# Performance work log

Measured on AMD Instinct MI355X. Metric: run time of the kernel, lower is better.

The kernel has to match this reference:

```python
import jax, jax.numpy as jnp
import numpy as np

B, N, C = 32, 577, 768
H = 12
D = C // H
HID = 4 * C
EPS = 1e-5


def setup_inputs() -> dict:
    key = jax.random.key(0)
    ks = jax.random.split(key, 12)
    s = 0.02
    return {
        "x": jax.random.normal(ks[0], (B, N, C), dtype=jnp.float32),
        "ln1_g": jnp.ones((C,), jnp.float32),
        "ln1_b": jnp.zeros((C,), jnp.float32),
        "qkv_w": jax.random.normal(ks[1], (C, 3 * C), jnp.float32) * s,
        "qkv_b": jnp.zeros((3 * C,), jnp.float32),
        "proj_w": jax.random.normal(ks[2], (C, C), jnp.float32) * s,
        "proj_b": jnp.zeros((C,), jnp.float32),
        "ln2_g": jnp.ones((C,), jnp.float32),
        "ln2_b": jnp.zeros((C,), jnp.float32),
        "fc1_w": jax.random.normal(ks[3], (C, HID), jnp.float32) * s,
        "fc1_b": jnp.zeros((HID,), jnp.float32),
        "fc2_w": jax.random.normal(ks[4], (HID, C), jnp.float32) * s,
        "fc2_b": jnp.zeros((C,), jnp.float32),
    }


def _layernorm(x, g, b):
    mu = jnp.mean(x, axis=-1, keepdims=True)
    var = jnp.mean(jnp.square(x - mu), axis=-1, keepdims=True)
    return (x - mu) * jax.lax.rsqrt(var + EPS) * g + b


def reference(x, ln1_g, ln1_b, qkv_w, qkv_b, proj_w, proj_b,
              ln2_g, ln2_b, fc1_w, fc1_b, fc2_w, fc2_b):
    b, n, c = x.shape
    # --- MSA branch ---
    h = _layernorm(x, ln1_g, ln1_b)
    qkv = h @ qkv_w + qkv_b                      # [b, n, 3c]
    qkv = qkv.reshape(b, n, 3, H, D).transpose(2, 0, 3, 1, 4)  # [3, b, h, n, d]
    q, k, v = qkv[0], qkv[1], qkv[2]
    scale = D ** -0.5
    attn = jnp.einsum('bhqd,bhkd->bhqk', q, k) * scale
    attn = jax.nn.softmax(attn, axis=-1)
    o = jnp.einsum('bhqk,bhkd->bhqd', attn, v)   # [b, h, n, d]
    o = o.transpose(0, 2, 1, 3).reshape(b, n, c)
    o = o @ proj_w + proj_b
    x = x + o
    # --- MLP branch ---
    h = _layernorm(x, ln2_g, ln2_b)
    h = jax.nn.gelu(h @ fc1_w + fc1_b, approximate=False)  # torch nn.GELU = exact erf
    h = h @ fc2_w + fc2_b
    return x + h
```

## Files before the change

### kernel.cpp

```cpp
#include <hip/hip_runtime.h>

typedef unsigned short u16;
typedef short short8 __attribute__((ext_vector_type(8)));
typedef float f32x4 __attribute__((ext_vector_type(4)));

#define MM 18464
#define NTOK 577

__device__ __forceinline__ u16 f2bf(float f) {
    unsigned u = __builtin_bit_cast(unsigned, f);
    u += 0x7fffu + ((u >> 16) & 1u);
    return (u16)(u >> 16);
}

__device__ __forceinline__ void gload16(const void* g, void* lds) {
    __builtin_amdgcn_global_load_lds(
        (const __attribute__((address_space(1))) unsigned*)g,
        (__attribute__((address_space(3))) unsigned*)lds,
        16, 0, 0);
}

__device__ __forceinline__ int xcd_map(int flat, int nwg) {
    const int q = nwg >> 3, r = nwg & 7;
    const int xcd = flat & 7, lid = flat >> 3;
    return (xcd < r ? xcd * (q + 1) : r * (q + 1) + (xcd - r) * q) + lid;
}

__device__ __forceinline__ int2 xcd_swz2(int gx, int gy) {
    const int w = xcd_map(blockIdx.x + blockIdx.y * gx, gx * gy);
    int2 o; o.x = w % gx; o.y = w / gx; return o;
}

__global__ __launch_bounds__(256) void convT(const float* __restrict__ src,
                                             u16* __restrict__ dst, int K, int N) {
    __shared__ float tile[32][33];
    const int k0 = blockIdx.x * 32, n0 = blockIdx.y * 32;
    const int tx = threadIdx.x & 31, ty = threadIdx.x >> 5;
#pragma unroll
    for (int i = 0; i < 32; i += 8)
        tile[ty + i][tx] = src[(size_t)(k0 + ty + i) * N + n0 + tx];
    __syncthreads();
#pragma unroll
    for (int i = 0; i < 32; i += 8)
        dst[(size_t)(n0 + ty + i) * K + k0 + tx] = f2bf(tile[tx][ty + i]);
}

__global__ __launch_bounds__(192) void ln_k(const float* __restrict__ x,
                                            const float* __restrict__ g,
                                            const float* __restrict__ bt,
                                            u16* __restrict__ out) {
    const int row = blockIdx.x, t = threadIdx.x;
    const float4 v = reinterpret_cast<const float4*>(x + (size_t)row * 768)[t];
    float s = v.x + v.y + v.z + v.w;
    float s2 = v.x * v.x + v.y * v.y + v.z * v.z + v.w * v.w;
#pragma unroll
    for (int off = 32; off > 0; off >>= 1) {
        s += __shfl_down(s, off);
        s2 += __shfl_down(s2, off);
    }
    __shared__ float red[6];
    if ((t & 63) == 0) { red[t >> 6] = s; red[3 + (t >> 6)] = s2; }
    __syncthreads();
    const float S = red[0] + red[1] + red[2];
    const float S2 = red[3] + red[4] + red[5];
    const float mu = S * (1.f / 768.f);
    const float var = S2 * (1.f / 768.f) - mu * mu;
    const float rs = rsqrtf(var + 1e-5f);
    const float4 gg = reinterpret_cast<const float4*>(g)[t];
    const float4 bb = reinterpret_cast<const float4*>(bt)[t];
    ushort4 r;
    r.x = f2bf((v.x - mu) * rs * gg.x + bb.x);
    r.y = f2bf((v.y - mu) * rs * gg.y + bb.y);
    r.z = f2bf((v.z - mu) * rs * gg.z + bb.z);
    r.w = f2bf((v.w - mu) * rs * gg.w + bb.w);
    reinterpret_cast<ushort4*>(out + (size_t)row * 768)[t] = r;
}

template <int MODE>
__global__ __launch_bounds__(512, 2) void gemm_k(const u16* __restrict__ A,
                                                 const u16* __restrict__ BT,
                                                 const float* __restrict__ bias,
                                                 const float* __restrict__ resid,
                                                 void* __restrict__ outp,
                                                 int M, int N, int K, int mt) {
    __shared__ u16 smem[4][256 * 64];
    const int t = threadIdx.x;
    const int wid = t >> 6, lane = t & 63;
    const int l15 = lane & 15, lg = lane >> 4;
    const int wr = wid >> 2, wc = wid & 3;

    const int w = xcd_map(blockIdx.x, gridDim.x);
    const int m0 = (w % mt) * 256, n0 = (w / mt) * 256;

    f32x4 acc[8][4] = {};
    const int NT = K >> 6;

    auto stage = [&](int buf, int k0) {
        u16* Ad = smem[buf * 2];
        u16* Bd = smem[buf * 2 + 1];
#pragma unroll
        for (int i = 0; i < 4; ++i) {
            const int slot = i * 512 + t;
            const int r = slot >> 3, sl = slot & 7;
            const int cs = (sl ^ (r & 7)) << 3;
            const size_t dofs = (size_t)(i * 512 + (t & ~63)) * 8;
            gload16(A + (size_t)min(m0 + r, M - 1) * K + k0 + cs, Ad + dofs);
            gload16(BT + (size_t)(n0 + r) * K + k0 + cs, Bd + dofs);
        }
    };

    auto compute = [&](int buf) {
        const u16* Ab = smem[buf * 2];
        const u16* Bb = smem[buf * 2 + 1];
#pragma unroll
        for (int half = 0; half < 2; ++half) {
            short8 af[8], bf4[4];
#pragma unroll
            for (int mf = 0; mf < 8; ++mf) {
                const int r = wr * 128 + mf * 16 + l15;
                af[mf] = *(const short8*)&Ab[r * 64 + (((half * 4 + lg) ^ (l15 & 7)) << 3)];
            }
#pragma unroll
            for (int nf = 0; nf < 4; ++nf) {
                const int r = wc * 64 + nf * 16 + l15;
                bf4[nf] = *(const short8*)&Bb[r * 64 + (((half * 4 + lg) ^ (l15 & 7)) << 3)];
            }
            __builtin_amdgcn_s_setprio(1);
#pragma unroll
            for (int mf = 0; mf < 8; ++mf)
#pragma unroll
                for (int nf = 0; nf < 4; ++nf)
                    acc[mf][nf] = __builtin_amdgcn_mfma_f32_16x16x32_bf16(
                        af[mf], bf4[nf], acc[mf][nf], 0, 0, 0);
            __builtin_amdgcn_s_setprio(0);
        }
    };

    stage(0, 0);
    stage(1, 64);
    for (int tt = 0; tt < NT; ++tt) {
        if (tt < NT - 1) asm volatile("s_waitcnt vmcnt(8)" ::: "memory");
        else             asm volatile("s_waitcnt vmcnt(0)" ::: "memory");
        __builtin_amdgcn_s_barrier();
        __builtin_amdgcn_sched_barrier(0);
        compute(tt & 1);
        __builtin_amdgcn_sched_barrier(0);
        asm volatile("s_waitcnt lgkmcnt(0)" ::: "memory");
        __builtin_amdgcn_s_barrier();
        __builtin_amdgcn_sched_barrier(0);
        if (tt + 2 < NT) stage(tt & 1, (tt + 2) << 6);
    }

    float bcol[4];
#pragma unroll
    for (int nf = 0; nf < 4; ++nf) bcol[nf] = bias[n0 + wc * 64 + nf * 16 + l15];
#pragma unroll
    for (int mf = 0; mf < 8; ++mf) {
#pragma unroll
        for (int reg = 0; reg < 4; ++reg) {
            const int row = m0 + wr * 128 + mf * 16 + lg * 4 + reg;
            if (row < M) {
#pragma unroll
                for (int nf = 0; nf < 4; ++nf) {
                    const int col = n0 + wc * 64 + nf * 16 + l15;
                    float v = acc[mf][nf][reg] + bcol[nf];
                    if (MODE == 2) v = 0.5f * v * (1.0f + erff(v * 0.70710678118f));
                    if (MODE == 1 || MODE == 3) v += resid[(size_t)row * N + col];
                    if (MODE == 0 || MODE == 2)
                        ((u16*)outp)[(size_t)row * N + col] = f2bf(v);
                    else
                        ((float*)outp)[(size_t)row * N + col] = v;
                }
            }
        }
    }
}

__global__ __launch_bounds__(256) void attn_k(const u16* __restrict__ qkv,
                                              u16* __restrict__ o) {
    const int2 sw = xcd_swz2(10, 384);
    const int qt = sw.x;
    const int bh = sw.y;
    const int b = bh / 12, h = bh % 12;
    const int t = threadIdx.x, wid = t >> 6, lane = t & 63;
    const int l15 = lane & 15, lg = lane >> 4;
    const size_t base = ((size_t)b * NTOK) * 2304 + (size_t)h * 64;

    __shared__ u16 Ks[64 * 64], VT[64 * 64], Ps[64 * 64];

    int qrow = qt * 64 + wid * 16 + l15;
    qrow = min(qrow, NTOK - 1);
    const u16* Qp = qkv + base + (size_t)qrow * 2304 + lg * 8;
    const short8 qf0 = *(const short8*)(Qp);
    const short8 qf1 = *(const short8*)(Qp + 32);

    f32x4 oacc[4] = {};
    float m_run[4], l_run[4];
#pragma unroll
    for (int j = 0; j < 4; ++j) { m_run[j] = -1e30f; l_run[j] = 0.f; }

    const int srow = t >> 3;
    const int cchunk = t & 7;
    const int ksd = (cchunk ^ (srow & 7)) * 8;
    u16* ldsK = Ks + wid * 512;
    const int vs0 = ((srow >> 3) ^ cchunk) * 8 + (srow & 7);
    const int vs1 = (((srow >> 3) + 4) ^ cchunk) * 8 + (srow & 7);

    for (int kt = 0; kt < 10; ++kt) {
        const int n0t = kt * 64;
        const int r0 = min(n0t + srow, NTOK - 1);
        const int r1 = min(n0t + srow + 32, NTOK - 1);
        gload16(qkv + base + 768 + (size_t)r0 * 2304 + ksd, ldsK);
        gload16(qkv + base + 768 + (size_t)r1 * 2304 + ksd, ldsK + 2048);
        const short8 v0 = *(const short8*)(qkv + base + 1536 + (size_t)r0 * 2304 + cchunk * 8);
        const short8 v1 = *(const short8*)(qkv + base + 1536 + (size_t)r1 * 2304 + cchunk * 8);
#pragma unroll
        for (int j = 0; j < 8; ++j) {
            VT[(cchunk * 8 + j) * 64 + vs0] = (u16)v0[j];
            VT[(cchunk * 8 + j) * 64 + vs1] = (u16)v1[j];
        }
        __syncthreads();

        f32x4 s[4];
#pragma unroll
        for (int fc = 0; fc < 4; ++fc) {
            const int krow = fc * 16 + l15;
            const short8 kf0 = *(const short8*)&Ks[krow * 64 + ((lg ^ (krow & 7)) * 8)];
            const short8 kf1 = *(const short8*)&Ks[krow * 64 + (((lg + 4) ^ (krow & 7)) * 8)];
            f32x4 a_ = {};
            a_ = __builtin_amdgcn_mfma_f32_16x16x32_bf16(qf0, kf0, a_, 0, 0, 0);
            a_ = __builtin_amdgcn_mfma_f32_16x16x32_bf16(qf1, kf1, a_, 0, 0, 0);
            s[fc] = a_;
        }
#pragma unroll
        for (int fc = 0; fc < 4; ++fc) {
            const bool valid = (n0t + fc * 16 + l15) < NTOK;
#pragma unroll
            for (int j = 0; j < 4; ++j)
                s[fc][j] = valid ? s[fc][j] * 0.125f : -1e30f;
        }
        float mt_[4];
#pragma unroll
        for (int j = 0; j < 4; ++j)
            mt_[j] = fmaxf(fmaxf(s[0][j], s[1][j]), fmaxf(s[2][j], s[3][j]));
#pragma unroll
        for (int off = 1; off < 16; off <<= 1)
#pragma unroll
            for (int j = 0; j < 4; ++j) mt_[j] = fmaxf(mt_[j], __shfl_xor(mt_[j], off));
        float mn[4], alpha[4];
#pragma unroll
        for (int j = 0; j < 4; ++j) {
            mn[j] = fmaxf(m_run[j], mt_[j]);
            alpha[j] = __expf(m_run[j] - mn[j]);
            m_run[j] = mn[j];
        }
        float lsum[4] = {0.f, 0.f, 0.f, 0.f};
#pragma unroll
        for (int fc = 0; fc < 4; ++fc)
#pragma unroll
            for (int j = 0; j < 4; ++j) {
                const float p = __expf(s[fc][j] - mn[j]);
                s[fc][j] = p;
                lsum[j] += p;
            }
#pragma unroll
        for (int off = 1; off < 16; off <<= 1)
#pragma unroll
            for (int j = 0; j < 4; ++j) lsum[j] += __shfl_xor(lsum[j], off);
#pragma unroll
        for (int j = 0; j < 4; ++j) l_run[j] = l_run[j] * alpha[j] + lsum[j];
#pragma unroll
        for (int fc = 0; fc < 4; ++fc)
#pragma unroll
            for (int j = 0; j < 4; ++j) oacc[fc][j] *= alpha[j];

#pragma unroll
        for (int fc = 0; fc < 4; ++fc)
#pragma unroll
            for (int j = 0; j < 4; ++j) {
                const int q = wid * 16 + lg * 4 + j;
                Ps[q * 64 + (((fc * 2 + (l15 >> 3)) ^ (q & 7)) * 8) + (l15 & 7)] =
                    f2bf(s[fc][j]);
            }
        asm volatile("s_waitcnt lgkmcnt(0)" ::: "memory");

#pragma unroll
        for (int c = 0; c < 2; ++c) {
            const short8 pf = *(const short8*)
                &Ps[(wid * 16 + l15) * 64 + (((c * 4 + lg) ^ (l15 & 7)) * 8)];
#pragma unroll
            for (int fc = 0; fc < 4; ++fc) {
                const short8 vf = *(const short8*)
                    &VT[(fc * 16 + l15) * 64 +
                        (((c * 4 + lg) ^ (fc * 2 + (l15 >> 3))) * 8)];
                oacc[fc] = __builtin_amdgcn_mfma_f32_16x16x32_bf16(pf, vf, oacc[fc], 0, 0, 0);
            }
        }
        __syncthreads();
    }

#pragma unroll
    for (int j = 0; j < 4; ++j) {
        const int row = qt * 64 + wid * 16 + lg * 4 + j;
        if (row < NTOK) {
            const float inv = 1.0f / l_run[j];
#pragma unroll
            for (int fc = 0; fc < 4; ++fc)
                o[((size_t)(b * NTOK + row)) * 768 + h * 64 + fc * 16 + l15] =
                    f2bf(oacc[fc][j] * inv);
        }
    }
}

extern "C" void kernel_launch(void* const* d_in, const int* in_sizes, int n_in,
                              void* d_out, int out_size, void* d_ws, size_t ws_size,
                              hipStream_t stream) {
    const float* x      = (const float*)d_in[0];
    const float* ln1_g  = (const float*)d_in[1];
    const float* ln1_b  = (const float*)d_in[2];
    const float* qkv_w  = (const float*)d_in[3];
    const float* qkv_b  = (const float*)d_in[4];
    const float* proj_w = (const float*)d_in[5];
    const float* proj_b = (const float*)d_in[6];
    const float* ln2_g  = (const float*)d_in[7];
    const float* ln2_b  = (const float*)d_in[8];
    const float* fc1_w  = (const float*)d_in[9];
    const float* fc1_b  = (const float*)d_in[10];
    const float* fc2_w  = (const float*)d_in[11];
    const float* fc2_b  = (const float*)d_in[12];
    float* out = (float*)d_out;

    char* ws = (char*)d_ws;
    size_t off = 0;
    u16* WQ  = (u16*)(ws + off); off += (size_t)2304 * 768 * 2;
    u16* WP  = (u16*)(ws + off); off += (size_t)768 * 768 * 2;
    u16* W1  = (u16*)(ws + off); off += (size_t)3072 * 768 * 2;
    u16* W2  = (u16*)(ws + off); off += (size_t)768 * 3072 * 2;
    u16* LN1 = (u16*)(ws + off); off += (size_t)MM * 768 * 2;
    u16* QKV = (u16*)(ws + off); off += (size_t)MM * 2304 * 2;
    u16* OB  = (u16*)(ws + off); off += (size_t)MM * 768 * 2;
    float* X1 = (float*)(ws + off); off += (size_t)MM * 768 * 4;
    u16* LN2 = (u16*)(ws + off); off += (size_t)MM * 768 * 2;
    u16* HID = LN1;

    convT<<<dim3(24, 72), 256, 0, stream>>>(qkv_w, WQ, 768, 2304);
    convT<<<dim3(24, 24), 256, 0, stream>>>(proj_w, WP, 768, 768);
    convT<<<dim3(24, 96), 256, 0, stream>>>(fc1_w, W1, 768, 3072);
    convT<<<dim3(96, 24), 256, 0, stream>>>(fc2_w, W2, 3072, 768);

    const int mt = (MM + 255) / 256;
    ln_k<<<MM, 192, 0, stream>>>(x, ln1_g, ln1_b, LN1);
    gemm_k<0><<<mt * 9, 512, 0, stream>>>(LN1, WQ, qkv_b, nullptr, QKV,
                                          MM, 2304, 768, mt);
    attn_k<<<dim3(10, 384), 256, 0, stream>>>(QKV, OB);
    gemm_k<1><<<mt * 3, 512, 0, stream>>>(OB, WP, proj_b, x, X1,
                                          MM, 768, 768, mt);
    ln_k<<<MM, 192, 0, stream>>>(X1, ln2_g, ln2_b, LN2);
    gemm_k<2><<<mt * 12, 512, 0, stream>>>(LN2, W1, fc1_b, nullptr, HID,
                                           MM, 3072, 768, mt);
    gemm_k<3><<<mt * 3, 512, 0, stream>>>(HID, W2, fc2_b, X1, out,
                                          MM, 768, 3072, mt);
}
```

Baseline: 749.6 us.

## Split GEMM k-tiles into half-planes with 4-phase interleaved load/compute pipeline

Restructures the bf16 GEMM main loop so each 64-wide k-tile is held as two 32-wide half planes per matrix. Each tile is processed in four phases, and every phase issues the global-to-LDS prefetch for the next tile while running MFMAs on the current one. The LDS swizzle is changed, and the MFMA operand order is swapped so each lane holds four consecutive output columns. That lets the epilogue use vectorized float4 bias and residual loads and ushort4/float4 stores. The cost is more barriers per tile and more complex wait-count bookkeeping.

Result: no change. 741.6 us (-1.1%).

```diff
diff --git a/kernel.cpp b/kernel.cpp
--- a/kernel.cpp
+++ b/kernel.cpp
@@ -83,93 +83,119 @@
                                                  const float* __restrict__ resid,
                                                  void* __restrict__ outp,
                                                  int M, int N, int K, int mt) {
-    __shared__ u16 smem[4][256 * 64];
+    __shared__ u16 smem[65536];
     const int t = threadIdx.x;
     const int wid = t >> 6, lane = t & 63;
     const int l15 = lane & 15, lg = lane >> 4;
     const int wr = wid >> 2, wc = wid & 3;
-
     const int w = xcd_map(blockIdx.x, gridDim.x);
     const int m0 = (w % mt) * 256, n0 = (w / mt) * 256;
+    const int swz = (l15 >> 1) & 3;
 
     f32x4 acc[8][4] = {};
     const int NT = K >> 6;
 
-    auto stage = [&](int buf, int k0) {
-        u16* Ad = smem[buf * 2];
-        u16* Bd = smem[buf * 2 + 1];
-#pragma unroll
-        for (int i = 0; i < 4; ++i) {
-            const int slot = i * 512 + t;
-            const int r = slot >> 3, sl = slot & 7;
-            const int cs = (sl ^ (r & 7)) << 3;
-            const size_t dofs = (size_t)(i * 512 + (t & ~63)) * 8;
-            gload16(A + (size_t)min(m0 + r, M - 1) * K + k0 + cs, Ad + dofs);
-            gload16(BT + (size_t)(n0 + r) * K + k0 + cs, Bd + dofs);
+    auto stage = [&](int buf, int kt, int mat, int kh) {
+        u16* plane = smem + (size_t)(((buf << 1) | mat) * 2 + kh) * 8192;
+        const u16* src = mat ? BT : A;
+        const int rbase = mat ? n0 : m0;
+        const int kk = kt * 64 + kh * 32;
+#pragma unroll
+        for (int i = 0; i < 2; ++i) {
+            const int flat = i * 512 + t;
+            const int r = flat >> 2, c = flat & 3;
+            const int scol = (c ^ ((r >> 1) & 3)) << 3;
+            int grow = rbase + r;
+            if (mat == 0) grow = min(grow, M - 1);
+            gload16(src + (size_t)grow * K + kk + scol,
+                    plane + (size_t)(i * 512 + (t & ~63)) * 8);
         }
     };
 
-    auto compute = [&](int buf) {
-        const u16* Ab = smem[buf * 2];
-        const u16* Bb = smem[buf * 2 + 1];
-#pragma unroll
-        for (int half = 0; half < 2; ++half) {
-            short8 af[8], bf4[4];
-#pragma unroll
-            for (int mf = 0; mf < 8; ++mf) {
-                const int r = wr * 128 + mf * 16 + l15;
-                af[mf] = *(const short8*)&Ab[r * 64 + (((half * 4 + lg) ^ (l15 & 7)) << 3)];
-            }
-#pragma unroll
-            for (int nf = 0; nf < 4; ++nf) {
-                const int r = wc * 64 + nf * 16 + l15;
-                bf4[nf] = *(const short8*)&Bb[r * 64 + (((half * 4 + lg) ^ (l15 & 7)) << 3)];
-            }
-            __builtin_amdgcn_s_setprio(1);
-#pragma unroll
-            for (int mf = 0; mf < 8; ++mf)
-#pragma unroll
-                for (int nf = 0; nf < 4; ++nf)
-                    acc[mf][nf] = __builtin_amdgcn_mfma_f32_16x16x32_bf16(
-                        af[mf], bf4[nf], acc[mf][nf], 0, 0, 0);
-            __builtin_amdgcn_s_setprio(0);
-        }
+    short8 bfv[4];
+    auto read_bf = [&](int buf, int kh) {
+        const u16* plane = smem + (size_t)((buf << 1 | 1) * 2 + kh) * 8192;
+        const int rb = wc * 64 + l15;
+#pragma unroll
+        for (int nf = 0; nf < 4; ++nf)
+            bfv[nf] = *(const short8*)&plane[(rb + nf * 16) * 32 + ((lg ^ swz) << 3)];
     };
-
-    stage(0, 0);
-    stage(1, 64);
-    for (int tt = 0; tt < NT; ++tt) {
-        if (tt < NT - 1) asm volatile("s_waitcnt vmcnt(8)" ::: "memory");
-        else             asm volatile("s_waitcnt vmcnt(0)" ::: "memory");
+    auto phase = [&](int buf, int mh, int kh, bool loadB,
+                     int stMat, int stKh, int kt1, bool doStage, int vm) {
+        if (loadB) read_bf(buf, kh);
+        short8 afv[4];
+        {
+            const u16* plane = smem + (size_t)((buf << 1) * 2 + kh) * 8192;
+            const int rb = wr * 128 + mh * 64 + l15;
+#pragma unroll
+            for (int mf = 0; mf < 4; ++mf)
+                afv[mf] = *(const short8*)&plane[(rb + mf * 16) * 32 + ((lg ^ swz) << 3)];
+        }
+        if (doStage) stage(buf ^ 1, kt1, stMat, stKh);
+        __builtin_amdgcn_s_barrier();
+        asm volatile("s_waitcnt lgkmcnt(0)" ::: "memory");
+        __builtin_amdgcn_sched_barrier(0);
+        __builtin_amdgcn_s_setprio(1);
+#pragma unroll
+        for (int mf = 0; mf < 4; ++mf)
+#pragma unroll
+            for (int nf = 0; nf < 4; ++nf)
+                acc[mh * 4 + mf][nf] = __builtin_amdgcn_mfma_f32_16x16x32_bf16(
+                    bfv[nf], afv[mf], acc[mh * 4 + mf][nf], 0, 0, 0);
+        __builtin_amdgcn_s_setprio(0);
+        if (vm == 4)      asm volatile("s_waitcnt vmcnt(4)" ::: "memory");
+        else if (vm == 0) asm volatile("s_waitcnt vmcnt(0)" ::: "memory");
         __builtin_amdgcn_s_barrier();
         __builtin_amdgcn_sched_barrier(0);
-        compute(tt & 1);
-        __builtin_amdgcn_sched_barrier(0);
-        asm volatile("s_waitcnt lgkmcnt(0)" ::: "memory");
-        __builtin_amdgcn_s_barrier();
-        __builtin_amdgcn_sched_barrier(0);
-        if (tt + 2 < NT) stage(tt & 1, (tt + 2) << 6);
-    }
-
-    float bcol[4];
-#pragma unroll
-    for (int nf = 0; nf < 4; ++nf) bcol[nf] = bias[n0 + wc * 64 + nf * 16 + l15];
+    };
+
+    stage(0, 0, 0, 0); stage(0, 0, 1, 0); stage(0, 0, 0, 1); stage(0, 0, 1, 1);
+    asm volatile("s_waitcnt vmcnt(4)" ::: "memory");
+    __builtin_amdgcn_s_barrier();
+    __builtin_amdgcn_sched_barrier(0);
+
+    int buf = 0;
+    for (int tt = 0; tt < NT; ++tt) {
+        const bool pre = (tt + 1 < NT);
+        phase(buf, 0, 0, true,  0, 0, tt + 1, pre, -1);
+        phase(buf, 1, 0, false, 1, 0, tt + 1, pre, pre ? 4 : 0);
+        phase(buf, 0, 1, true,  0, 1, tt + 1, pre, -1);
+        phase(buf, 1, 1, false, 1, 1, tt + 1, pre, pre ? 4 : -1);
+        buf ^= 1;
+    }
+
+    float4 bb4[4];
+#pragma unroll
+    for (int nf = 0; nf < 4; ++nf)
+        bb4[nf] = *(const float4*)&bias[n0 + wc * 64 + nf * 16 + lg * 4];
 #pragma unroll
     for (int mf = 0; mf < 8; ++mf) {
-#pragma unroll
-        for (int reg = 0; reg < 4; ++reg) {
-            const int row = m0 + wr * 128 + mf * 16 + lg * 4 + reg;
-            if (row < M) {
-#pragma unroll
-                for (int nf = 0; nf < 4; ++nf) {
-                    const int col = n0 + wc * 64 + nf * 16 + l15;
-                    float v = acc[mf][nf][reg] + bcol[nf];
-                    if (MODE == 2) v = 0.5f * v * (1.0f + erff(v * 0.70710678118f));
-                    if (MODE == 1 || MODE == 3) v += resid[(size_t)row * N + col];
-                    if (MODE == 0 || MODE == 2)
-                        ((u16*)outp)[(size_t)row * N + col] = f2bf(v);
-                    else
-                        ((float*)outp)[(size_t)row * N + col] = v;
+        const int row = m0 + wr * 128 + mf * 16 + l15;
+        if (row < M) {
+#pragma unroll
+            for (int nf = 0; nf < 4; ++nf) {
+                const int col = n0 + wc * 64 + nf * 16 + lg * 4;
+                float v0 = acc[mf][nf][0] + bb4[nf].x;
+                float v1 = acc[mf][nf][1] + bb4[nf].y;
+                float v2 = acc[mf][nf][2] + bb4[nf].z;
+                float v3 = acc[mf][nf][3] + bb4[nf].w;
+                if (MODE == 2) {
+                    v0 = 0.5f * v0 * (1.0f + erff(v0 * 0.70710678118f));
+                    v1 = 0.5f * v1 * (1.0f + erff(v1 * 0.70710678118f));
+                    v2 = 0.5f * v2 * (1.0f + erff(v2 * 0.70710678118f));
+                    v3 = 0.5f * v3 * (1.0f + erff(v3 * 0.70710678118f));
+                }
+                if (MODE == 1 || MODE == 3) {
+                    const float4 rr = *(const float4*)&resid[(size_t)row * N + col];
+                    v0 += rr.x; v1 += rr.y; v2 += rr.z; v3 += rr.w;
+                }
+                if (MODE == 0 || MODE == 2) {
+                    ushort4 r4;
+                    r4.x = f2bf(v0); r4.y = f2bf(v1); r4.z = f2bf(v2); r4.w = f2bf(v3);
+                    *(ushort4*)&((u16*)outp)[(size_t)row * N + col] = r4;
+                } else {
+                    float4 f4; f4.x = v0; f4.y = v1; f4.z = v2; f4.w = v3;
+                    *(float4*)&((float*)outp)[(size_t)row * N + col] = f4;
                 }
             }
         }
```

## Restructure GEMM main loop into half-K stages with interleaved prefetch and LDS epilogue

Applied to the files above, without the earlier changes.

Rewrites the GEMM mainloop so each 64-wide K tile is split into two 32-wide sub-tiles, with global-to-LDS prefetch of the next tile issued between MFMA groups instead of after a full barrier. Precomputed load pointers and a new swizzle cut address arithmetic, and the A/B operand order in the MFMA is swapped. The epilogue now transposes accumulators through padded LDS, so bias, GELU, residual and stores use float4/ushort4 vector accesses instead of scalar ones. The goal is better overlap of memory and matrix work and coalesced stores, at the cost of more complex synchronization and a risk of LDS hazards.

After: 817.7 us. 9.1% more time.

```diff
diff --git a/kernel.cpp b/kernel.cpp
--- a/kernel.cpp
+++ b/kernel.cpp
@@ -83,93 +83,156 @@
                                                  const float* __restrict__ resid,
                                                  void* __restrict__ outp,
                                                  int M, int N, int K, int mt) {
-    __shared__ u16 smem[4][256 * 64];
+    __shared__ u16 smem[65536];
     const int t = threadIdx.x;
     const int wid = t >> 6, lane = t & 63;
     const int l15 = lane & 15, lg = lane >> 4;
     const int wr = wid >> 2, wc = wid & 3;
-
     const int w = xcd_map(blockIdx.x, gridDim.x);
     const int m0 = (w % mt) * 256, n0 = (w / mt) * 256;
+    const int swz = (l15 >> 1) & 3;
+
+    const int rs = t >> 2;
+    const int scol = ((t & 3) ^ ((rs >> 1) & 3)) << 3;
+    const u16* aP0 = A + (size_t)min(m0 + rs, M - 1) * K + scol;
+    const u16* aP1 = A + (size_t)min(m0 + rs + 128, M - 1) * K + scol;
+    const u16* bP0 = BT + (size_t)(n0 + rs) * K + scol;
+    const u16* bP1 = BT + (size_t)(n0 + rs + 128) * K + scol;
+    const int d0 = (t & ~63) * 8, d1 = 4096 + (t & ~63) * 8;
+
+    const int aRd = (wr * 128 + l15) * 32 + ((lg ^ swz) << 3);
+    const int bRd = (wc * 64 + l15) * 32 + ((lg ^ swz) << 3);
 
     f32x4 acc[8][4] = {};
     const int NT = K >> 6;
 
-    auto stage = [&](int buf, int k0) {
-        u16* Ad = smem[buf * 2];
-        u16* Bd = smem[buf * 2 + 1];
-#pragma unroll
-        for (int i = 0; i < 4; ++i) {
-            const int slot = i * 512 + t;
-            const int r = slot >> 3, sl = slot & 7;
-            const int cs = (sl ^ (r & 7)) << 3;
-            const size_t dofs = (size_t)(i * 512 + (t & ~63)) * 8;
-            gload16(A + (size_t)min(m0 + r, M - 1) * K + k0 + cs, Ad + dofs);
-            gload16(BT + (size_t)(n0 + r) * K + k0 + cs, Bd + dofs);
-        }
+    auto stA = [&](int pb, int kk) {
+        gload16(aP0 + kk, smem + pb + d0);
+        gload16(aP1 + kk, smem + pb + d1);
     };
-
-    auto compute = [&](int buf) {
-        const u16* Ab = smem[buf * 2];
-        const u16* Bb = smem[buf * 2 + 1];
-#pragma unroll
-        for (int half = 0; half < 2; ++half) {
-            short8 af[8], bf4[4];
-#pragma unroll
-            for (int mf = 0; mf < 8; ++mf) {
-                const int r = wr * 128 + mf * 16 + l15;
-                af[mf] = *(const short8*)&Ab[r * 64 + (((half * 4 + lg) ^ (l15 & 7)) << 3)];
-            }
-#pragma unroll
-            for (int nf = 0; nf < 4; ++nf) {
-                const int r = wc * 64 + nf * 16 + l15;
-                bf4[nf] = *(const short8*)&Bb[r * 64 + (((half * 4 + lg) ^ (l15 & 7)) << 3)];
-            }
-            __builtin_amdgcn_s_setprio(1);
-#pragma unroll
-            for (int mf = 0; mf < 8; ++mf)
-#pragma unroll
-                for (int nf = 0; nf < 4; ++nf)
-                    acc[mf][nf] = __builtin_amdgcn_mfma_f32_16x16x32_bf16(
-                        af[mf], bf4[nf], acc[mf][nf], 0, 0, 0);
-            __builtin_amdgcn_s_setprio(0);
-        }
+    auto stB = [&](int pb, int kk) {
+        gload16(bP0 + kk, smem + pb + d0);
+        gload16(bP1 + kk, smem + pb + d1);
     };
 
-    stage(0, 0);
-    stage(1, 64);
-    for (int tt = 0; tt < NT; ++tt) {
-        if (tt < NT - 1) asm volatile("s_waitcnt vmcnt(8)" ::: "memory");
-        else             asm volatile("s_waitcnt vmcnt(0)" ::: "memory");
+    auto tile = [&](int pb, int kkn, bool pre, bool last) {
+        short8 bfv[4], afv[4];
+#pragma unroll
+        for (int nf = 0; nf < 4; ++nf)
+            bfv[nf] = *(const short8*)&smem[pb + 16384 + bRd + nf * 512];
+#pragma unroll
+        for (int mf = 0; mf < 4; ++mf)
+            afv[mf] = *(const short8*)&smem[pb + aRd + mf * 512];
+        if (pre) stA(pb ^ 32768, kkn);
+        __builtin_amdgcn_s_setprio(1);
+#pragma unroll
+        for (int mf = 0; mf < 4; ++mf)
+#pragma unroll
+            for (int nf = 0; nf < 4; ++nf)
+                acc[mf][nf] = __builtin_amdgcn_mfma_f32_16x16x32_bf16(
+                    bfv[nf], afv[mf], acc[mf][nf], 0, 0, 0);
+        __builtin_amdgcn_s_setprio(0);
+#pragma unroll
+        for (int mf = 0; mf < 4; ++mf)
+            afv[mf] = *(const short8*)&smem[pb + aRd + 2048 + mf * 512];
+        if (pre) stB((pb ^ 32768) + 16384, kkn);
+        __builtin_amdgcn_s_setprio(1);
+#pragma unroll
+        for (int mf = 0; mf < 4; ++mf)
+#pragma unroll
+            for (int nf = 0; nf < 4; ++nf)
+                acc[4 + mf][nf] = __builtin_amdgcn_mfma_f32_16x16x32_bf16(
+                    bfv[nf], afv[mf], acc[4 + mf][nf], 0, 0, 0);
+        __builtin_amdgcn_s_setprio(0);
+        if (last) asm volatile("s_waitcnt vmcnt(0)" ::: "memory");
+        else      asm volatile("s_waitcnt vmcnt(4)" ::: "memory");
         __builtin_amdgcn_s_barrier();
         __builtin_amdgcn_sched_barrier(0);
-        compute(tt & 1);
-        __builtin_amdgcn_sched_barrier(0);
+#pragma unroll
+        for (int nf = 0; nf < 4; ++nf)
+            bfv[nf] = *(const short8*)&smem[pb + 16384 + 8192 + bRd + nf * 512];
+#pragma unroll
+        for (int mf = 0; mf < 4; ++mf)
+            afv[mf] = *(const short8*)&smem[pb + 8192 + aRd + mf * 512];
+        if (pre) stA((pb ^ 32768) + 8192, kkn + 32);
+        __builtin_amdgcn_s_setprio(1);
+#pragma unroll
+        for (int mf = 0; mf < 4; ++mf)
+#pragma unroll
+            for (int nf = 0; nf < 4; ++nf)
+                acc[mf][nf] = __builtin_amdgcn_mfma_f32_16x16x32_bf16(
+                    bfv[nf], afv[mf], acc[mf][nf], 0, 0, 0);
+        __builtin_amdgcn_s_setprio(0);
+#pragma unroll
+        for (int mf = 0; mf < 4; ++mf)
+            afv[mf] = *(const short8*)&smem[pb + 8192 + aRd + 2048 + mf * 512];
+        if (pre) stB((pb ^ 32768) + 16384 + 8192, kkn + 32);
+        __builtin_amdgcn_s_setprio(1);
+#pragma unroll
+        for (int mf = 0; mf < 4; ++mf)
+#pragma unroll
+            for (int nf = 0; nf < 4; ++nf)
+                acc[4 + mf][nf] = __builtin_amdgcn_mfma_f32_16x16x32_bf16(
+                    bfv[nf], afv[mf], acc[4 + mf][nf], 0, 0, 0);
+        __builtin_amdgcn_s_setprio(0);
+        if (pre) {
+            asm volatile("s_waitcnt vmcnt(4)" ::: "memory");
+            __builtin_amdgcn_s_barrier();
+            __builtin_amdgcn_sched_barrier(0);
+        }
+    };
+
+    stA(0, 0); stB(16384, 0);
+    __builtin_amdgcn_sched_barrier(0);
+    stA(8192, 32); stB(16384 + 8192, 32);
+    asm volatile("s_waitcnt vmcnt(4)" ::: "memory");
+    __builtin_amdgcn_s_barrier();
+    __builtin_amdgcn_sched_barrier(0);
+
+    int kkn = 64;
+    const int half = NT >> 1;
+    for (int it = 0; it < half; ++it) {
+        tile(0, kkn, true, false);
+        kkn += 64;
+        const bool pre = (it + 1 < half);
+        tile(32768, kkn, pre, !pre);
+        kkn += 64;
+    }
+
+    __syncthreads();
+    const int col = n0 + wc * 64 + l15 * 4;
+    const float4 bias4 = *(const float4*)&bias[col];
+#pragma unroll
+    for (int mf = 0; mf < 8; ++mf) {
+        float* ws_ = (float*)smem + wid * 2144 + (mf & 1) * 1072;
         asm volatile("s_waitcnt lgkmcnt(0)" ::: "memory");
-        __builtin_amdgcn_s_barrier();
-        __builtin_amdgcn_sched_barrier(0);
-        if (tt + 2 < NT) stage(tt & 1, (tt + 2) << 6);
-    }
-
-    float bcol[4];
-#pragma unroll
-    for (int nf = 0; nf < 4; ++nf) bcol[nf] = bias[n0 + wc * 64 + nf * 16 + l15];
-#pragma unroll
-    for (int mf = 0; mf < 8; ++mf) {
-#pragma unroll
-        for (int reg = 0; reg < 4; ++reg) {
-            const int row = m0 + wr * 128 + mf * 16 + lg * 4 + reg;
-            if (row < M) {
-#pragma unroll
-                for (int nf = 0; nf < 4; ++nf) {
-                    const int col = n0 + wc * 64 + nf * 16 + l15;
-                    float v = acc[mf][nf][reg] + bcol[nf];
-                    if (MODE == 2) v = 0.5f * v * (1.0f + erff(v * 0.70710678118f));
-                    if (MODE == 1 || MODE == 3) v += resid[(size_t)row * N + col];
-                    if (MODE == 0 || MODE == 2)
-                        ((u16*)outp)[(size_t)row * N + col] = f2bf(v);
-                    else
-                        ((float*)outp)[(size_t)row * N + col] = v;
+#pragma unroll
+        for (int nf = 0; nf < 4; ++nf)
+            *(f32x4*)&ws_[l15 * 67 + nf * 16 + lg * 4] = acc[mf][nf];
+#pragma unroll
+        for (int ps = 0; ps < 4; ++ps) {
+            const int rl = ps * 4 + lg;
+            float4 v = *(const float4*)&ws_[rl * 67 + l15 * 4];
+            v.x += bias4.x; v.y += bias4.y; v.z += bias4.z; v.w += bias4.w;
+            if (MODE == 2) {
+                v.x = 0.5f * v.x * (1.0f + erff(v.x * 0.70710678118f));
+                v.y = 0.5f * v.y * (1.0f + erff(v.y * 0.70710678118f));
+                v.z = 0.5f * v.z * (1.0f + erff(v.z * 0.70710678118f));
+                v.w = 0.5f * v.w * (1.0f + erff(v.w * 0.70710678118f));
+            }
+            const int grow = m0 + wr * 128 + mf * 16 + rl;
+            if (grow < M) {
+                if (MODE == 1 || MODE == 3) {
+                    const float4 rr = *(const float4*)&resid[(size_t)grow * N + col];
+                    v.x += rr.x; v.y += rr.y; v.z += rr.z; v.w += rr.w;
+                }
+                if (MODE == 0 || MODE == 2) {
+                    ushort4 r4;
+                    r4.x = f2bf(v.x); r4.y = f2bf(v.y);
+                    r4.z = f2bf(v.z); r4.w = f2bf(v.w);
+                    *(ushort4*)&((u16*)outp)[(size_t)grow * N + col] = r4;
+                } else {
+                    *(float4*)&((float*)outp)[(size_t)grow * N + col] = v;
                 }
             }
         }
```
